# Optimization experiments

Hardware: AMD Instinct MI355X
Metric: run time of the kernel (lower is better)

The kernel has to match this reference:

```python
import jax, jax.numpy as jnp
import numpy as np


def setup_inputs() -> dict:
    key = jax.random.key(0)
    ks = jax.random.split(key, 18)
    B, T, L, C = 16, 512, 50, 7
    H = 512
    s = 0.05
    inp = {
        "phone_data": jax.random.normal(ks[0], (B, T, L, C), jnp.float32),
        "h0": jax.random.normal(ks[1], (B, H), jnp.float32),
        "conv1_w": jax.random.normal(ks[2], (128, 7, 11), jnp.float32) * s,
        "conv1_b": jax.random.normal(ks[3], (128,), jnp.float32) * s,
        "conv2_w": jax.random.normal(ks[4], (256, 128, 9), jnp.float32) * s,
        "conv2_b": jax.random.normal(ks[5], (256,), jnp.float32) * s,
        "fc1_w": jax.random.normal(ks[6], (1024, 1536), jnp.float32) * s,
        "fc1_b": jax.random.normal(ks[7], (1024,), jnp.float32) * s,
        "fc2_w": jax.random.normal(ks[8], (512, 1024), jnp.float32) * s,
        "fc2_b": jax.random.normal(ks[9], (512,), jnp.float32) * s,
        "gru_wih": jax.random.normal(ks[10], (3 * H, H), jnp.float32) * s,
        "gru_whh": jax.random.normal(ks[11], (3 * H, H), jnp.float32) * s,
        "gru_bih": jax.random.normal(ks[12], (3 * H,), jnp.float32) * s,
        "gru_bhh": jax.random.normal(ks[13], (3 * H,), jnp.float32) * s,
        "fc3_w": jax.random.normal(ks[14], (1, H), jnp.float32) * s,
        "fc3_b": jax.random.normal(ks[15], (1,), jnp.float32) * s,
    }
    return inp


def reference(phone_data, h0, conv1_w, conv1_b, conv2_w, conv2_b,
              fc1_w, fc1_b, fc2_w, fc2_b,
              gru_wih, gru_whh, gru_bih, gru_bhh, fc3_w, fc3_b):
    B, T, L, C = phone_data.shape
    N = B * T
    # ---- batched CNN + FC feature extractor (independent per frame) ----
    x = phone_data.reshape(N, L, C).transpose(0, 2, 1)  # [N, 7, 50]
    y = jax.lax.conv_general_dilated(
        x, conv1_w, (1,), 'VALID',
        dimension_numbers=('NCH', 'OIH', 'NCH')) + conv1_b[None, :, None]  # [N,128,40]
    y = y.reshape(N, 128, 20, 2).max(-1)  # maxpool k=2,s=2 -> [N,128,20]
    y = jax.lax.conv_general_dilated(
        y, conv2_w, (1,), 'VALID',
        dimension_numbers=('NCH', 'OIH', 'NCH')) + conv2_b[None, :, None]  # [N,256,12]
    y = y.reshape(N, 256, 6, 2).max(-1)  # [N,256,6]
    feat = y.reshape(N, 1536)            # Flatten(0): channel-major, matches torch
    feat = feat @ fc1_w.T + fc1_b        # [N,1024]
    feat = feat @ fc2_w.T + fc2_b        # [N,512]
    feat = feat.reshape(B, T, 512)

    # ---- sequential GRUCell recurrence (PyTorch GRUCell math) ----
    def cell(h, x_t):
        gi = x_t @ gru_wih.T + gru_bih   # [B, 3H]
        gh = h @ gru_whh.T + gru_bhh     # [B, 3H]
        ir, iz, in_ = jnp.split(gi, 3, axis=-1)
        hr, hz, hn = jnp.split(gh, 3, axis=-1)
        r = jax.nn.sigmoid(ir + hr)
        z = jax.nn.sigmoid(iz + hz)
        n = jnp.tanh(in_ + r * hn)
        h_new = (1 - z) * n + z * h
        # original code calls hx.detach() every step
        h_new = jax.lax.stop_gradient(h_new)
        return h_new, h_new

    _, hs = jax.lax.scan(cell, h0, feat.transpose(1, 0, 2))  # hs: [T,B,512]
    out = hs @ fc3_w.T + fc3_b  # [T,B,1]
    return out.transpose(1, 0, 2)  # [B,T,1]
```

## Files before the change

kernel.cpp:

```cpp
#include <hip/hip_runtime.h>
#include <hip/hip_bf16.h>
#include <math.h>
#include <stdint.h>

typedef __attribute__((ext_vector_type(8))) short short8;
typedef __attribute__((ext_vector_type(4))) float f32x4;
typedef __attribute__((ext_vector_type(4))) unsigned int uint4v;

#define T_ 512

__device__ __forceinline__ unsigned short bf16rn(float f) {
  union { float f; unsigned u; } x; x.f = f;
  unsigned r = x.u + 0x7FFF + ((x.u >> 16) & 1);
  return (unsigned short)(r >> 16);
}

__device__ __forceinline__ void gload16(const void* gsrc, void* ldst) {
  __builtin_amdgcn_global_load_lds(
      (const __attribute__((address_space(1))) unsigned int*)gsrc,
      (__attribute__((address_space(3))) unsigned int*)ldst, 16, 0, 0);
}

__global__ __launch_bounds__(256) void conv1_kernel(
    const float* __restrict__ phone, const float* __restrict__ w1,
    const float* __restrict__ b1, ushort* __restrict__ out1b) {
  __shared__ float ws[128 * 77];
  __shared__ float bs[128];
  __shared__ float xs[8][7][52];
  const int tid = threadIdx.x;
  const int n0 = blockIdx.x * 8;
  for (int idx = tid; idx < 9856; idx += 256) ws[idx] = w1[idx];
  if (tid < 128) bs[tid] = b1[tid];
  for (int idx = tid; idx < 2800; idx += 256) {
    int fi = idx / 350, r = idx - fi * 350;
    int ll = r / 7, c = r - ll * 7;
    xs[fi][c][ll] = phone[(size_t)(n0 + fi) * 350 + r];
  }
  __syncthreads();

  const int o = tid >> 1, ph = tid & 1;
  const float* wo = ws + o * 77;
  const float bb = bs[o];
  for (int fi = 0; fi < 8; ++fi) {
    float acc0[10], acc1[10];
#pragma unroll
    for (int q = 0; q < 10; ++q) { acc0[q] = 0.f; acc1[q] = 0.f; }
    for (int i = 0; i < 7; ++i) {
      float wr[11];
#pragma unroll
      for (int k = 0; k < 11; ++k) wr[k] = wo[i * 11 + k];
#pragma unroll
      for (int q = 0; q < 10; ++q) {
        int p = ph * 10 + q;
        int base = 2 * p;
        float xv[12];
#pragma unroll
        for (int j = 0; j < 12; ++j) xv[j] = xs[fi][i][base + j];
        float s0 = 0.f, s1 = 0.f;
#pragma unroll
        for (int k = 0; k < 11; ++k) {
          s0 += xv[k] * wr[k];
          s1 += xv[k + 1] * wr[k];
        }
        acc0[q] += s0;
        acc1[q] += s1;
      }
    }
#pragma unroll
    for (int q = 0; q < 10; ++q) {
      int p = ph * 10 + q;
      out1b[((size_t)(n0 + fi) * 128 + o) * 20 + p] =
          bf16rn(fmaxf(acc0[q], acc1[q]) + bb);
    }
  }
}

__global__ __launch_bounds__(256) void f32_to_bf16(
    const float* __restrict__ src, ushort* __restrict__ dst, int n4) {
  int i = blockIdx.x * 256 + threadIdx.x;
  if (i < n4) {
    float4 v = ((const float4*)src)[i];
    ushort4 o;
    o.x = bf16rn(v.x); o.y = bf16rn(v.y); o.z = bf16rn(v.z); o.w = bf16rn(v.w);
    ((ushort4*)dst)[i] = o;
  }
}

__global__ __launch_bounds__(256) void stage_h0(
    const float* __restrict__ h0, unsigned long long* __restrict__ hxt) {
  const int tid = threadIdx.x;
  const int b = tid >> 4, x = tid & 15;
#pragma unroll
  for (int q = 0; q < 16; ++q) {
    int d = (x + q * 16) * 2;
    int s = d >> 5, fqq = (d >> 3) & 3, k = (d & 7) >> 1;
    int lane = b | (fqq << 4);
    float2 h2 = *(const float2*)(h0 + (size_t)b * 512 + d);
    unsigned pk = (unsigned)bf16rn(h2.x) | ((unsigned)bf16rn(h2.y) << 16);
    hxt[((size_t)s * 64 + lane) * 4 + k] = (unsigned long long)pk;
  }
}

template <int AM, int EM>
__global__ __launch_bounds__(256) void gemm_bf16(
    const ushort* __restrict__ A, const ushort* __restrict__ W,
    const float* __restrict__ bias, void* __restrict__ Cout,
    int K, int lda, int ldc) {
  __shared__ ushort As[128 * 64];
  __shared__ ushort Bs[128 * 64];
  const int tid = threadIdx.x;
  const int l = tid & 63, wv = tid >> 6;
  const int wr = wv >> 1, wc = wv & 1;
  const int fr = l & 15, fq = l >> 4;
  const int bm0 = blockIdx.x * 128, bn0 = blockIdx.y * 128;

  f32x4 acc[4][4];
#pragma unroll
  for (int mi = 0; mi < 4; ++mi)
#pragma unroll
    for (int ni = 0; ni < 4; ++ni) acc[mi][ni] = (f32x4)0.f;

  const int pr8 = l >> 3;
  const int pc = l & 7;
  const int nkt = K >> 6;
  for (int kt = 0; kt < nkt; ++kt) {
    const int k0 = kt << 6;
#pragma unroll
    for (int i = 0; i < 4; ++i) {
      int q = wv * 4 + i;
      int prow = q * 8 + pr8;
      int lc = pc ^ (prow & 7);
      gload16(W + (size_t)(bn0 + prow) * K + k0 + lc * 8, &Bs[q * 512]);
    }
    if (AM == 0) {
#pragma unroll
      for (int i = 0; i < 4; ++i) {
        int q = wv * 4 + i;
        int prow = q * 8 + pr8;
        int lc = pc ^ (prow & 7);
        gload16(A + (size_t)(bm0 + prow) * lda + k0 + lc * 8, &As[q * 512]);
      }
    } else {
#pragma unroll
      for (int q = 0; q < 16; ++q) {
        int idx = tid + q * 256;
        int row = idx >> 5, c0 = (idx & 31) * 2;
        int m = bm0 + row;
        int n = m / 12, pos = m - n * 12;
        int kk = k0 + c0;
        int i2 = kk / 9, kp = kk - i2 * 9;
        uint e0 = A[(size_t)n * 2560 + i2 * 20 + pos + kp];
        int kk1 = kk + 1;
        int i3 = kk1 / 9, kp1 = kk1 - i3 * 9;
        uint e1 = A[(size_t)n * 2560 + i3 * 20 + pos + kp1];
        *(uint*)&As[row * 64 + (((c0 >> 3) ^ (row & 7)) << 3) + (c0 & 7)] =
            e0 | (e1 << 16);
      }
    }
    __syncthreads();
#pragma unroll
    for (int ks = 0; ks < 2; ++ks) {
      short8 af[4], bfr[4];
#pragma unroll
      for (int mi = 0; mi < 4; ++mi) {
        int row = wr * 64 + mi * 16 + fr;
        af[mi] = *(const short8*)&As[row * 64 + (((ks * 4 + fq) ^ (row & 7)) << 3)];
      }
#pragma unroll
      for (int ni = 0; ni < 4; ++ni) {
        int row = wc * 64 + ni * 16 + fr;
        bfr[ni] = *(const short8*)&Bs[row * 64 + (((ks * 4 + fq) ^ (row & 7)) << 3)];
      }
#pragma unroll
      for (int mi = 0; mi < 4; ++mi)
#pragma unroll
        for (int ni = 0; ni < 4; ++ni)
          acc[mi][ni] = __builtin_amdgcn_mfma_f32_16x16x32_bf16(
              af[mi], bfr[ni], acc[mi][ni], 0, 0, 0);
    }
    __syncthreads();
  }

#pragma unroll
  for (int ni = 0; ni < 4; ++ni) {
    int col = bn0 + wc * 64 + ni * 16 + fr;
    float bv = bias[col];
#pragma unroll
    for (int mi = 0; mi < 4; ++mi) {
      int mbase = bm0 + wr * 64 + mi * 16 + fq * 4;
      if (EM == 0) {
        ushort* C = (ushort*)Cout;
#pragma unroll
        for (int j = 0; j < 4; ++j)
          C[(size_t)(mbase + j) * ldc + col] = bf16rn(acc[mi][ni][j] + bv);
      } else if (EM == 1) {
        ushort* C = (ushort*)Cout;
#pragma unroll
        for (int j = 0; j < 4; j += 2) {
          int m = mbase + j;
          int n = m / 12, pos = m - n * 12;
          float v = fmaxf(acc[mi][ni][j], acc[mi][ni][j + 1]) + bv;
          C[(size_t)n * 1536 + col * 6 + (pos >> 1)] = bf16rn(v);
        }
      } else {
        float* C = (float*)Cout;
#pragma unroll
        for (int j = 0; j < 4; ++j) {
          int m = mbase + j;
          int b = m >> 9, tt = m & 511;
          C[((size_t)tt * 16 + b) * 1536 + col] = acc[mi][ni][j] + bv;
        }
      }
    }
  }
}

__global__ __launch_bounds__(384) void gru_persistent(
    const float* __restrict__ h0, const float* __restrict__ gi,
    const float* __restrict__ whh, const float* __restrict__ bhh,
    float* __restrict__ hsbuf, unsigned long long* __restrict__ hxt) {
  __shared__ float gh_lds[6 * 256];
  __shared__ unsigned afl[16 * 64 * 4];
  const int tid = threadIdx.x;
  const int w = blockIdx.x;
  const int l = tid & 63, v = tid >> 6;
  const int fr = l & 15, fq = l >> 4;
  const int g = v >> 1, half = v & 1;
  const int o = g * 512 + w * 32 + half * 16 + fr;

  short8 bfrag[16];
#pragma unroll
  for (int s = 0; s < 16; ++s) {
    const float* wp = whh + (size_t)o * 512 + s * 32 + fq * 8;
    float4 w0 = *(const float4*)wp;
    float4 w1 = *(const float4*)(wp + 4);
    short8 bb;
    bb[0] = (short)bf16rn(w0.x); bb[1] = (short)bf16rn(w0.y);
    bb[2] = (short)bf16rn(w0.z); bb[3] = (short)bf16rn(w0.w);
    bb[4] = (short)bf16rn(w1.x); bb[5] = (short)bf16rn(w1.y);
    bb[6] = (short)bf16rn(w1.z); bb[7] = (short)bf16rn(w1.w);
    bfrag[s] = bb;
  }
  const float bo = bhh[o];

  const int b = tid >> 4, jp = tid & 15, jl = jp * 2;
  const bool gthr = (tid < 256);
  const int lane0 = jp * 4;
  float hA = 0.f, hB = 0.f;
  float giC0 = 0.f, giC1 = 0.f, giC2 = 0.f, giC3 = 0.f, giC4 = 0.f, giC5 = 0.f;
  float giN0 = 0.f, giN1 = 0.f, giN2 = 0.f, giN3 = 0.f, giN4 = 0.f, giN5 = 0.f;
  if (gthr) {
    float2 h2 = *(const float2*)(h0 + (size_t)b * 512 + w * 32 + jl);
    hA = h2.x; hB = h2.y;
    const float* gb = gi + (size_t)b * 1536 + w * 32 + jl;
    float2 r0 = *(const float2*)(gb);
    float2 r1 = *(const float2*)(gb + 512);
    float2 r2 = *(const float2*)(gb + 1024);
    giC0 = r0.x; giC3 = r0.y; giC1 = r1.x; giC4 = r1.y; giC2 = r2.x; giC5 = r2.y;
  }

  for (int t = 0; t < T_; ++t) {
    if (gthr) {
      const unsigned long long* src =
          hxt + (((size_t)(t & 1) * 16 + b) * 64 + lane0) * 4;
      uint4v r[8];
      for (;;) {
#pragma unroll
        for (int q = 0; q < 8; ++q)
          asm volatile("global_load_dwordx4 %0, %1, off sc0 sc1"
                       : "=v"(r[q]) : "v"(src + q * 2));
        asm volatile("s_waitcnt vmcnt(0)" ::: "memory");
        __builtin_amdgcn_sched_barrier(0);
        bool ok = true;
#pragma unroll
        for (int q = 0; q < 8; ++q)
          ok = ok & (r[q].y == (unsigned)t) & (r[q].w == (unsigned)t);
        if (ok) break;
      }
#pragma unroll
      for (int q = 0; q < 8; ++q) {
        uint2 d2 = make_uint2(r[q].x, r[q].z);
        *(uint2*)&afl[(b * 64 + lane0 + (q >> 1)) * 4 + (q & 1) * 2] = d2;
      }
      if (t > 0)
        *(float2*)(hsbuf + ((size_t)(t - 1) * 16 + b) * 512 + w * 32 + jl) =
            make_float2(hA, hB);
      if (t + 1 < T_) {
        const float* gb = gi + ((size_t)(t + 1) * 16 + b) * 1536 + w * 32 + jl;
        float2 r0 = *(const float2*)(gb);
        float2 r1 = *(const float2*)(gb + 512);
        float2 r2 = *(const float2*)(gb + 1024);
        giN0 = r0.x; giN3 = r0.y; giN1 = r1.x; giN4 = r1.y; giN2 = r2.x; giN5 = r2.y;
      }
    }
    __syncthreads();
    f32x4 a0 = (f32x4)0.f, a1 = (f32x4)0.f, a2 = (f32x4)0.f, a3 = (f32x4)0.f;
#pragma unroll
    for (int s = 0; s < 4; ++s) {
      union { uint4v u; short8 s8; } c0, c1, c2, c3;
      c0.u = *(const uint4v*)&afl[((4 * s + 0) * 64 + l) * 4];
      c1.u = *(const uint4v*)&afl[((4 * s + 1) * 64 + l) * 4];
      c2.u = *(const uint4v*)&afl[((4 * s + 2) * 64 + l) * 4];
      c3.u = *(const uint4v*)&afl[((4 * s + 3) * 64 + l) * 4];
      a0 = __builtin_amdgcn_mfma_f32_16x16x32_bf16(c0.s8, bfrag[4 * s + 0], a0, 0, 0, 0);
      a1 = __builtin_amdgcn_mfma_f32_16x16x32_bf16(c1.s8, bfrag[4 * s + 1], a1, 0, 0, 0);
      a2 = __builtin_amdgcn_mfma_f32_16x16x32_bf16(c2.s8, bfrag[4 * s + 2], a2, 0, 0, 0);
      a3 = __builtin_amdgcn_mfma_f32_16x16x32_bf16(c3.s8, bfrag[4 * s + 3], a3, 0, 0, 0);
    }
#pragma unroll
    for (int j = 0; j < 4; ++j)
      gh_lds[v * 256 + (fq * 4 + j) * 16 + fr] = a0[j] + a1[j] + a2[j] + a3[j] + bo;
    __syncthreads();
    if (gthr) {
      const int hh = jl >> 4, c = jl & 15;
      float2 rr = *(const float2*)&gh_lds[(0 + hh) * 256 + b * 16 + c];
      float2 zz = *(const float2*)&gh_lds[(2 + hh) * 256 + b * 16 + c];
      float2 nn = *(const float2*)&gh_lds[(4 + hh) * 256 + b * 16 + c];
      float rgA = __builtin_amdgcn_rcpf(1.f + __expf(-(giC0 + rr.x)));
      float rgB = __builtin_amdgcn_rcpf(1.f + __expf(-(giC3 + rr.y)));
      float zgA = __builtin_amdgcn_rcpf(1.f + __expf(-(giC1 + zz.x)));
      float zgB = __builtin_amdgcn_rcpf(1.f + __expf(-(giC4 + zz.y)));
      float eA = __expf(2.f * (giC2 + rgA * nn.x));
      float eB = __expf(2.f * (giC5 + rgB * nn.y));
      float ngA = 1.f - 2.f * __builtin_amdgcn_rcpf(eA + 1.f);
      float ngB = 1.f - 2.f * __builtin_amdgcn_rcpf(eB + 1.f);
      hA = (1.f - zgA) * ngA + zgA * hA;
      hB = (1.f - zgB) * ngB + zgB * hB;
      unsigned pk = (unsigned)bf16rn(hA) | ((unsigned)bf16rn(hB) << 16);
      unsigned long long payload =
          (unsigned long long)pk | ((unsigned long long)(unsigned)(t + 1) << 32);
      unsigned long long* dst =
          hxt + (((size_t)((t + 1) & 1) * 16 + w) * 64 + (b | ((jp >> 2) << 4))) * 4 +
          (jp & 3);
      __hip_atomic_store(dst, payload, __ATOMIC_RELAXED, __HIP_MEMORY_SCOPE_AGENT);
      giC0 = giN0; giC1 = giN1; giC2 = giN2;
      giC3 = giN3; giC4 = giN4; giC5 = giN5;
    }
  }
  if (gthr)
    *(float2*)(hsbuf + ((size_t)(T_ - 1) * 16 + b) * 512 + w * 32 + jl) =
        make_float2(hA, hB);
}

__global__ __launch_bounds__(256) void fc3_kernel(
    const float* __restrict__ hs, const float* __restrict__ w3,
    const float* __restrict__ b3, float* __restrict__ out) {
  __shared__ float w[512];
  const int tid = threadIdx.x;
  w[tid] = w3[tid];
  w[tid + 256] = w3[tid + 256];
  __syncthreads();
  const int gidx = blockIdx.x * 256 + tid;
  const int b = gidx >> 9, t = gidx & 511;
  const float4* hr = (const float4*)(hs + ((size_t)t * 16 + b) * 512);
  const float4* wr = (const float4*)w;
  float acc = 0.f;
#pragma unroll 8
  for (int kc = 0; kc < 128; ++kc) {
    float4 h = hr[kc], ww = wr[kc];
    acc += h.x * ww.x + h.y * ww.y + h.z * ww.z + h.w * ww.w;
  }
  out[gidx] = acc + b3[0];
}

extern "C" void kernel_launch(void* const* d_in, const int* in_sizes, int n_in,
                              void* d_out, int out_size, void* d_ws,
                              size_t ws_size, hipStream_t stream) {
  const float* phone = (const float*)d_in[0];
  const float* h0    = (const float*)d_in[1];
  const float* w1    = (const float*)d_in[2];
  const float* b1    = (const float*)d_in[3];
  const float* w2    = (const float*)d_in[4];
  const float* b2    = (const float*)d_in[5];
  const float* fc1w  = (const float*)d_in[6];
  const float* fc1b  = (const float*)d_in[7];
  const float* fc2w  = (const float*)d_in[8];
  const float* fc2b  = (const float*)d_in[9];
  const float* wih   = (const float*)d_in[10];
  const float* whh   = (const float*)d_in[11];
  const float* bih   = (const float*)d_in[12];
  const float* bhh   = (const float*)d_in[13];
  const float* w3    = (const float*)d_in[14];
  const float* b3    = (const float*)d_in[15];
  float* out = (float*)d_out;

  char* ws = (char*)d_ws;
  ushort* out1b = (ushort*)(ws + 0);
  ushort* feat2 = (ushort*)(ws + 41943040);
  ushort* feat3 = (ushort*)(ws + 67108864);
  ushort* feat4 = (ushort*)(ws + 83886080);
  float*  gibuf = (float*) (ws + 92274688);
  float*  hsbuf = (float*) (ws + 142606336);
  ushort* w2b   = (ushort*)(ws + 159383552);
  ushort* fc1wb = (ushort*)(ws + 159973376);
  ushort* fc2wb = (ushort*)(ws + 163119104);
  ushort* wihb  = (ushort*)(ws + 164167680);
  unsigned long long* hxt = (unsigned long long*)(ws + 67108864);

  f32_to_bf16<<<288, 256, 0, stream>>>(w2, w2b, 73728);
  f32_to_bf16<<<1536, 256, 0, stream>>>(fc1w, fc1wb, 393216);
  f32_to_bf16<<<512, 256, 0, stream>>>(fc2w, fc2wb, 131072);
  f32_to_bf16<<<768, 256, 0, stream>>>(wih, wihb, 196608);

  conv1_kernel<<<1024, 256, 0, stream>>>(phone, w1, b1, out1b);
  gemm_bf16<1, 1><<<dim3(768, 2), 256, 0, stream>>>(out1b, w2b, b2, feat2, 1152, 0, 0);
  gemm_bf16<0, 0><<<dim3(64, 8), 256, 0, stream>>>(feat2, fc1wb, fc1b, feat3, 1536, 1536, 1024);
  gemm_bf16<0, 0><<<dim3(64, 4), 256, 0, stream>>>(feat3, fc2wb, fc2b, feat4, 1024, 1024, 512);
  gemm_bf16<0, 2><<<dim3(64, 12), 256, 0, stream>>>(feat4, wihb, bih, gibuf, 512, 512, 1536);

  hipMemsetAsync(hxt, 0, 32768, stream);
  stage_h0<<<1, 256, 0, stream>>>(h0, hxt);
  gru_persistent<<<16, 384, 0, stream>>>(h0, gibuf, whh, bhh, hsbuf, hxt);

  fc3_kernel<<<32, 256, 0, stream>>>(hsbuf, w3, b3, out);
}
```

Measured before the change: 1.838 ms.

## Move GRU hidden-state polling to spare warps and precompute im2col index table

```diff
diff --git a/kernel.cpp b/kernel.cpp
--- a/kernel.cpp
+++ b/kernel.cpp
@@ -108,11 +108,20 @@
     int K, int lda, int ldc) {
   __shared__ ushort As[128 * 64];
   __shared__ ushort Bs[128 * 64];
+  __shared__ ushort tbl[1152];
   const int tid = threadIdx.x;
   const int l = tid & 63, wv = tid >> 6;
   const int wr = wv >> 1, wc = wv & 1;
   const int fr = l & 15, fq = l >> 4;
   const int bm0 = blockIdx.x * 128, bn0 = blockIdx.y * 128;
+
+  if (AM == 1) {
+    for (int idx = tid; idx < 1152; idx += 256) {
+      int i2 = idx / 9, kp = idx - i2 * 9;
+      tbl[idx] = (ushort)(i2 * 20 + kp);
+    }
+    __syncthreads();
+  }
 
   f32x4 acc[4][4];
 #pragma unroll
@@ -148,11 +157,9 @@
         int m = bm0 + row;
         int n = m / 12, pos = m - n * 12;
         int kk = k0 + c0;
-        int i2 = kk / 9, kp = kk - i2 * 9;
-        uint e0 = A[(size_t)n * 2560 + i2 * 20 + pos + kp];
-        int kk1 = kk + 1;
-        int i3 = kk1 / 9, kp1 = kk1 - i3 * 9;
-        uint e1 = A[(size_t)n * 2560 + i3 * 20 + pos + kp1];
+        const ushort* an = A + (size_t)n * 2560 + pos;
+        uint e0 = an[tbl[kk]];
+        uint e1 = an[tbl[kk + 1]];
         *(uint*)&As[row * 64 + (((c0 >> 3) ^ (row & 7)) << 3) + (c0 & 7)] =
             e0 | (e1 << 16);
       }
@@ -245,55 +252,48 @@
 
   const int b = tid >> 4, jp = tid & 15, jl = jp * 2;
   const bool gthr = (tid < 256);
-  const int lane0 = jp * 4;
+  const int pt = tid - 256;
   float hA = 0.f, hB = 0.f;
   float giC0 = 0.f, giC1 = 0.f, giC2 = 0.f, giC3 = 0.f, giC4 = 0.f, giC5 = 0.f;
   float giN0 = 0.f, giN1 = 0.f, giN2 = 0.f, giN3 = 0.f, giN4 = 0.f, giN5 = 0.f;
   if (gthr) {
     float2 h2 = *(const float2*)(h0 + (size_t)b * 512 + w * 32 + jl);
     hA = h2.x; hB = h2.y;
-    const float* gb = gi + (size_t)b * 1536 + w * 32 + jl;
-    float2 r0 = *(const float2*)(gb);
-    float2 r1 = *(const float2*)(gb + 512);
-    float2 r2 = *(const float2*)(gb + 1024);
+    const float* g0 = gi + (size_t)b * 1536 + w * 32 + jl;
+    float2 r0 = *(const float2*)(g0);
+    float2 r1 = *(const float2*)(g0 + 512);
+    float2 r2 = *(const float2*)(g0 + 1024);
     giC0 = r0.x; giC3 = r0.y; giC1 = r1.x; giC4 = r1.y; giC2 = r2.x; giC5 = r2.y;
-  }
+    const float* g1 = gi + (size_t)(16 + b) * 1536 + w * 32 + jl;
+    float2 s0 = *(const float2*)(g1);
+    float2 s1 = *(const float2*)(g1 + 512);
+    float2 s2 = *(const float2*)(g1 + 1024);
+    giN0 = s0.x; giN3 = s0.y; giN1 = s1.x; giN4 = s1.y; giN2 = s2.x; giN5 = s2.y;
+  }
+
+  if (!gthr) {
+    const unsigned long long* base = hxt + pt * 2;
+    uint4v r[16];
+    for (;;) {
+#pragma unroll
+      for (int m = 0; m < 16; ++m)
+        asm volatile("global_load_dwordx4 %0, %1, off sc0 sc1"
+                     : "=v"(r[m]) : "v"(base + m * 256));
+      asm volatile("s_waitcnt vmcnt(0)" ::: "memory");
+      __builtin_amdgcn_sched_barrier(0);
+      bool ok = true;
+#pragma unroll
+      for (int m = 0; m < 16; ++m)
+        ok = ok & (r[m].y == 0u) & (r[m].w == 0u);
+      if (ok) break;
+    }
+#pragma unroll
+    for (int m = 0; m < 16; ++m)
+      *(uint2*)&afl[pt * 2 + m * 256] = make_uint2(r[m].x, r[m].z);
+  }
+  __syncthreads();
 
   for (int t = 0; t < T_; ++t) {
-    if (gthr) {
-      const unsigned long long* src =
-          hxt + (((size_t)(t & 1) * 16 + b) * 64 + lane0) * 4;
-      uint4v r[8];
-      for (;;) {
-#pragma unroll
-        for (int q = 0; q < 8; ++q)
-          asm volatile("global_load_dwordx4 %0, %1, off sc0 sc1"
-                       : "=v"(r[q]) : "v"(src + q * 2));
-        asm volatile("s_waitcnt vmcnt(0)" ::: "memory");
-        __builtin_amdgcn_sched_barrier(0);
-        bool ok = true;
-#pragma unroll
-        for (int q = 0; q < 8; ++q)
-          ok = ok & (r[q].y == (unsigned)t) & (r[q].w == (unsigned)t);
-        if (ok) break;
-      }
-#pragma unroll
-      for (int q = 0; q < 8; ++q) {
-        uint2 d2 = make_uint2(r[q].x, r[q].z);
-        *(uint2*)&afl[(b * 64 + lane0 + (q >> 1)) * 4 + (q & 1) * 2] = d2;
-      }
-      if (t > 0)
-        *(float2*)(hsbuf + ((size_t)(t - 1) * 16 + b) * 512 + w * 32 + jl) =
-            make_float2(hA, hB);
-      if (t + 1 < T_) {
-        const float* gb = gi + ((size_t)(t + 1) * 16 + b) * 1536 + w * 32 + jl;
-        float2 r0 = *(const float2*)(gb);
-        float2 r1 = *(const float2*)(gb + 512);
-        float2 r2 = *(const float2*)(gb + 1024);
-        giN0 = r0.x; giN3 = r0.y; giN1 = r1.x; giN4 = r1.y; giN2 = r2.x; giN5 = r2.y;
-      }
-    }
-    __syncthreads();
     f32x4 a0 = (f32x4)0.f, a1 = (f32x4)0.f, a2 = (f32x4)0.f, a3 = (f32x4)0.f;
 #pragma unroll
     for (int s = 0; s < 4; ++s) {
@@ -311,6 +311,7 @@
     for (int j = 0; j < 4; ++j)
       gh_lds[v * 256 + (fq * 4 + j) * 16 + fr] = a0[j] + a1[j] + a2[j] + a3[j] + bo;
     __syncthreads();
+
     if (gthr) {
       const int hh = jl >> 4, c = jl & 15;
       float2 rr = *(const float2*)&gh_lds[(0 + hh) * 256 + b * 16 + c];
@@ -326,20 +327,50 @@
       float ngB = 1.f - 2.f * __builtin_amdgcn_rcpf(eB + 1.f);
       hA = (1.f - zgA) * ngA + zgA * hA;
       hB = (1.f - zgB) * ngB + zgB * hB;
-      unsigned pk = (unsigned)bf16rn(hA) | ((unsigned)bf16rn(hB) << 16);
-      unsigned long long payload =
-          (unsigned long long)pk | ((unsigned long long)(unsigned)(t + 1) << 32);
-      unsigned long long* dst =
-          hxt + (((size_t)((t + 1) & 1) * 16 + w) * 64 + (b | ((jp >> 2) << 4))) * 4 +
-          (jp & 3);
-      __hip_atomic_store(dst, payload, __ATOMIC_RELAXED, __HIP_MEMORY_SCOPE_AGENT);
+      if (t + 1 < T_) {
+        unsigned pk = (unsigned)bf16rn(hA) | ((unsigned)bf16rn(hB) << 16);
+        unsigned long long payload =
+            (unsigned long long)pk | ((unsigned long long)(unsigned)(t + 1) << 32);
+        unsigned long long* dst =
+            hxt + (((size_t)((t + 1) & 1) * 16 + w) * 64 + (b | ((jp >> 2) << 4))) * 4 +
+            (jp & 3);
+        __hip_atomic_store(dst, payload, __ATOMIC_RELAXED, __HIP_MEMORY_SCOPE_AGENT);
+      }
+      *(float2*)(hsbuf + ((size_t)t * 16 + b) * 512 + w * 32 + jl) =
+          make_float2(hA, hB);
       giC0 = giN0; giC1 = giN1; giC2 = giN2;
       giC3 = giN3; giC4 = giN4; giC5 = giN5;
-    }
-  }
-  if (gthr)
-    *(float2*)(hsbuf + ((size_t)(T_ - 1) * 16 + b) * 512 + w * 32 + jl) =
-        make_float2(hA, hB);
+      if (t + 2 < T_) {
+        const float* gb = gi + ((size_t)(t + 2) * 16 + b) * 1536 + w * 32 + jl;
+        float2 r0 = *(const float2*)(gb);
+        float2 r1 = *(const float2*)(gb + 512);
+        float2 r2 = *(const float2*)(gb + 1024);
+        giN0 = r0.x; giN3 = r0.y; giN1 = r1.x; giN4 = r1.y; giN2 = r2.x; giN5 = r2.y;
+      }
+    } else if (t + 1 < T_) {
+      const unsigned long long* base =
+          hxt + (size_t)((t + 1) & 1) * 4096 + pt * 2;
+      const unsigned tag = (unsigned)(t + 1);
+      uint4v r[16];
+      for (;;) {
+#pragma unroll
+        for (int m = 0; m < 16; ++m)
+          asm volatile("global_load_dwordx4 %0, %1, off sc0 sc1"
+                       : "=v"(r[m]) : "v"(base + m * 256));
+        asm volatile("s_waitcnt vmcnt(0)" ::: "memory");
+        __builtin_amdgcn_sched_barrier(0);
+        bool ok = true;
+#pragma unroll
+        for (int m = 0; m < 16; ++m)
+          ok = ok & (r[m].y == tag) & (r[m].w == tag);
+        if (ok) break;
+      }
+#pragma unroll
+      for (int m = 0; m < 16; ++m)
+        *(uint2*)&afl[pt * 2 + m * 256] = make_uint2(r[m].x, r[m].z);
+    }
+    __syncthreads();
+  }
 }
 
 __global__ __launch_bounds__(256) void fc3_kernel(
@@ -408,7 +439,7 @@
   gemm_bf16<0, 0><<<dim3(64, 4), 256, 0, stream>>>(feat3, fc2wb, fc2b, feat4, 1024, 1024, 512);
   gemm_bf16<0, 2><<<dim3(64, 12), 256, 0, stream>>>(feat4, wihb, bih, gibuf, 512, 512, 1536);
 
-  hipMemsetAsync(hxt, 0, 32768, stream);
+  hipMemsetAsync(hxt, 0, 65536, stream);
   stage_h0<<<1, 256, 0, stream>>>(h0, hxt);
   gru_persistent<<<16, 384, 0, stream>>>(h0, gibuf, whh, bhh, hsbuf, hxt);
 
```

After: 1.599 ms. 1.15x faster.
